# Kernel tuning notes

Measured on AMD Instinct MI355X. Metric: run time of the kernel, lower is better.

## Reference

```python
import jax, jax.numpy as jnp
import numpy as np

N = 100000        # number of nodes
E = 3200000       # number of edges (avg degree 32)
D_IN = 256
D_OUT = 256


def setup_inputs() -> dict:
    key = jax.random.key(0)
    k_x, k_w, k_r, k_c, k_v = jax.random.split(key, 5)
    x = jax.random.normal(k_x, (N, D_IN), dtype=jnp.float32)
    # nn.Linear weight, stored torch-style as (out_features, in_features)
    W = jax.random.normal(k_w, (D_OUT, D_IN), dtype=jnp.float32) / np.sqrt(D_IN)
    edge_row = jax.random.randint(k_r, (E,), 0, N, dtype=jnp.int32)
    edge_col = jax.random.randint(k_c, (E,), 0, N, dtype=jnp.int32)
    edge_val = jax.random.uniform(k_v, (E,), dtype=jnp.float32)
    return {"x": x, "W": W, "edge_row": edge_row, "edge_col": edge_col,
            "edge_val": edge_val}


def reference(x, W, edge_row, edge_col, edge_val):
    # support = X @ W^T  (torch nn.Linear, no bias), computed in float32
    support = jnp.einsum('nd,od->no', x.astype(jnp.float32), W.astype(jnp.float32))
    # SpMM: out[i] = sum_{e: row[e]==i} val[e] * support[col[e]]
    gathered = edge_val.astype(jnp.float32)[:, None] * support[edge_col]  # [E, D_OUT]
    out = jax.ops.segment_sum(gathered, edge_row, num_segments=N)        # [N, D_OUT]
    return out
```

## Files before the change

### kernel.cpp

```cpp
#include <hip/hip_runtime.h>

#define N_NODES 100000
#define N_EDGES 3200000
#define D 256

#define NBKT 391
#define BCAP 9216
#define P1_BLOCKS 782
#define GEMM_BLOCKS 1563
#define CVT_BLOCKS 64

using bf16x8 = __attribute__((ext_vector_type(8))) short;
using f32x4  = __attribute__((ext_vector_type(4))) float;
using i32x4  = __attribute__((ext_vector_type(4))) int;
using i32x2  = __attribute__((ext_vector_type(2))) int;

__device__ inline float bf2f(unsigned short b) {
    union { unsigned u; float f; } v; v.u = ((unsigned)b) << 16; return v.f;
}
__device__ inline unsigned short f2bf(float f) {
    union { float f; unsigned u; } v; v.f = f;
    unsigned u = v.u;
    u += 0x7FFFu + ((u >> 16) & 1u);
    return (unsigned short)(u >> 16);
}

__global__ __launch_bounds__(256) void prep(const float* __restrict__ W,
                                            unsigned short* __restrict__ wb,
                                            int* __restrict__ bucket_next) {
    int bid = blockIdx.x;
    if (bid < CVT_BLOCKS) {
        int i = (bid * 256 + threadIdx.x) * 4;
        float4 f = *(const float4*)(W + i);
        ushort4 o;
        o.x = f2bf(f.x); o.y = f2bf(f.y); o.z = f2bf(f.z); o.w = f2bf(f.w);
        *(ushort4*)(wb + i) = o;
    } else {
        int t = (bid - CVT_BLOCKS) * 256 + threadIdx.x;
        if (t < NBKT) bucket_next[t] = t * BCAP;
    }
}

__global__ __launch_bounds__(256) void gemm_part(
    const float* __restrict__ x,
    const unsigned short* __restrict__ wb,
    unsigned short* __restrict__ sb,
    const i32x4* __restrict__ erow4,
    const i32x4* __restrict__ ecol4,
    const f32x4* __restrict__ eval4,
    int* __restrict__ bucket_next,
    i32x2* __restrict__ bkt)
{
    __shared__ int h_cnt[NBKT];
    __shared__ int h_base[NBKT];
    int bid = blockIdx.x;
    int r3 = bid % 3, g3 = bid / 3;
    if (r3 == 0) {
        int p = g3;
        int tid = threadIdx.x;
        for (int i = tid; i < NBKT; i += 256) h_cnt[i] = 0;
        __syncthreads();
        int e0 = p * 4096;
        int jmax = (N_EDGES - e0) >> 10; if (jmax > 4) jmax = 4;
        int w0[4][4], w1[4][4], bs[4][4];
#pragma unroll
        for (int j = 0; j < 4; ++j) {
            if (j < jmax) {
                int q = p * 1024 + j * 256 + tid;
                i32x4 r4 = __builtin_nontemporal_load(erow4 + q);
                i32x4 c4 = __builtin_nontemporal_load(ecol4 + q);
                f32x4 v4 = __builtin_nontemporal_load(eval4 + q);
#pragma unroll
                for (int k = 0; k < 4; ++k) {
                    int row = r4[k];
                    int b   = row >> 8;
                    int rl  = row & 255;
                    int slot = atomicAdd(&h_cnt[b], 1);
                    w0[j][k] = c4[k] | (rl << 24);
                    w1[j][k] = __float_as_int(v4[k]);
                    bs[j][k] = (b << 14) | slot;
                }
            }
        }
        __syncthreads();
        for (int i = tid; i < NBKT; i += 256)
            h_base[i] = atomicAdd(&bucket_next[i], h_cnt[i]);
        __syncthreads();
#pragma unroll
        for (int j = 0; j < 4; ++j) {
            if (j < jmax) {
#pragma unroll
                for (int k = 0; k < 4; ++k) {
                    int b    = bs[j][k] >> 14;
                    int slot = bs[j][k] & 16383;
                    int dst  = h_base[b] + slot;
                    if (dst < (b + 1) * BCAP) {
                        i32x2 o; o[0] = w0[j][k]; o[1] = w1[j][k];
                        bkt[dst] = o;
                    }
                }
            }
        }
        return;
    }
    int g = 2 * g3 + (r3 - 1);
    int wave = g * 4 + (int)(threadIdx.x >> 6);
    int m0 = wave << 4;
    if (m0 >= N_NODES) return;
    int lane = threadIdx.x & 63;
    int quad = lane >> 4;
    int r16  = lane & 15;

    const f32x4* arow = (const f32x4*)(x + (size_t)(m0 + r16) * D + quad * 8);
    const unsigned short* bbase = wb + (size_t)r16 * D + quad * 8;

    f32x4 acc[16];
#pragma unroll
    for (int t = 0; t < 16; ++t) acc[t] = (f32x4){0.f, 0.f, 0.f, 0.f};

    for (int k0 = 0; k0 < D; k0 += 32) {
        f32x4 fa0 = __builtin_nontemporal_load(arow + (k0 >> 2));
        f32x4 fa1 = __builtin_nontemporal_load(arow + (k0 >> 2) + 1);
        bf16x8 a;
        a[0] = (short)f2bf(fa0[0]); a[1] = (short)f2bf(fa0[1]);
        a[2] = (short)f2bf(fa0[2]); a[3] = (short)f2bf(fa0[3]);
        a[4] = (short)f2bf(fa1[0]); a[5] = (short)f2bf(fa1[1]);
        a[6] = (short)f2bf(fa1[2]); a[7] = (short)f2bf(fa1[3]);
#pragma unroll
        for (int t = 0; t < 16; ++t) {
            bf16x8 b = *(const bf16x8*)(bbase + (size_t)t * 16 * D + k0);
            acc[t] = __builtin_amdgcn_mfma_f32_16x16x32_bf16(b, a, acc[t], 0, 0, 0);
        }
    }

#pragma unroll
    for (int t = 0; t < 16; ++t) {
        ushort4 o;
        o.x = f2bf(acc[t][0]); o.y = f2bf(acc[t][1]);
        o.z = f2bf(acc[t][2]); o.w = f2bf(acc[t][3]);
        *(ushort4*)(sb + (size_t)(m0 + r16) * D + t * 16 + quad * 4) = o;
    }
}

__global__ __launch_bounds__(1024) void build_csr(
    const int* __restrict__ bucket_next,
    i32x2* __restrict__ bkt,
    int* __restrict__ rowptr, int* __restrict__ cntout)
{
    __shared__ int cnt[256];
    __shared__ int scn[256];
    int b = blockIdx.x;
    int tid = threadIdx.x;
    int base = b * BCAP;
    int ne = bucket_next[b] - base; if (ne > BCAP) ne = BCAP;

    if (tid < 256) cnt[tid] = 0;
    __syncthreads();

    int w0[9], w1[9], sp[9];
#pragma unroll
    for (int j = 0; j < 9; ++j) {
        int idx = j * 1024 + tid;
        sp[j] = -1;
        if (idx < ne) {
            i32x2 e = bkt[base + idx];
            w0[j] = e[0]; w1[j] = e[1];
            int rl = ((unsigned)e[0]) >> 24;
            int s  = atomicAdd(&cnt[rl], 1);
            sp[j] = (rl << 16) | s;
        }
    }
    __syncthreads();
    if (tid < 256) scn[tid] = cnt[tid];
    __syncthreads();
    for (int off = 1; off < 256; off <<= 1) {
        int v = 0;
        if (tid < 256 && tid >= off) v = scn[tid - off];
        __syncthreads();
        if (tid < 256) scn[tid] += v;
        __syncthreads();
    }
    if (tid < 256) {
        int excl = scn[tid] - cnt[tid];
        scn[tid] = excl;
        int row = (b << 8) + tid;
        if (row < N_NODES) {
            rowptr[row] = base + excl;
            cntout[row] = cnt[tid];
        }
    }
    __syncthreads();
#pragma unroll
    for (int j = 0; j < 9; ++j) {
        if (sp[j] >= 0) {
            int rl = sp[j] >> 16, s = sp[j] & 0xFFFF;
            i32x2 o; o[0] = w0[j] & 0x00FFFFFF; o[1] = w1[j];
            bkt[base + scn[rl] + s] = o;
        }
    }
}

__global__ __launch_bounds__(256) void spmm_gather(
    const int* __restrict__ rowptr, const int* __restrict__ cntout,
    const i32x2* __restrict__ csr,
    const unsigned short* __restrict__ sb, float* __restrict__ out)
{
    int wave = (int)((blockIdx.x * 256u + threadIdx.x) >> 6);
    if (wave >= N_NODES) return;
    int lane = threadIdx.x & 63;
    int hi = lane >> 5;
    const unsigned short* base = sb + (size_t)(lane & 31) * 8;

    int beg = rowptr[wave];
    int end = beg + cntout[wave];

    f32x4 a0 = {0.f,0.f,0.f,0.f}, b0 = {0.f,0.f,0.f,0.f};
    f32x4 a1 = {0.f,0.f,0.f,0.f}, b1 = {0.f,0.f,0.f,0.f};
    f32x4 a2 = {0.f,0.f,0.f,0.f}, b2 = {0.f,0.f,0.f,0.f};
    f32x4 a3 = {0.f,0.f,0.f,0.f}, b3 = {0.f,0.f,0.f,0.f};

#define PAIR(AA, BB, EE) do {                                        \
        i32x2 pa = __builtin_nontemporal_load(csr + (EE));           \
        i32x2 pb = __builtin_nontemporal_load(csr + (EE) + 1);       \
        int   col = hi ? pb[0] : pa[0];                              \
        float v   = __int_as_float(hi ? pb[1] : pa[1]);              \
        bf16x8 s = *(const bf16x8*)(base + ((size_t)col << 8));      \
        AA[0] += v * bf2f((unsigned short)s[0]);                     \
        AA[1] += v * bf2f((unsigned short)s[1]);                     \
        AA[2] += v * bf2f((unsigned short)s[2]);                     \
        AA[3] += v * bf2f((unsigned short)s[3]);                     \
        BB[0] += v * bf2f((unsigned short)s[4]);                     \
        BB[1] += v * bf2f((unsigned short)s[5]);                     \
        BB[2] += v * bf2f((unsigned short)s[6]);                     \
        BB[3] += v * bf2f((unsigned short)s[7]);                     \
    } while (0)

    int e = beg;
    for (; e + 8 <= end; e += 8) {
        PAIR(a0, b0, e);
        PAIR(a1, b1, e + 2);
        PAIR(a2, b2, e + 4);
        PAIR(a3, b3, e + 6);
    }
    for (; e + 2 <= end; e += 2) PAIR(a0, b0, e);
    if (e < end) {
        i32x2 pa = __builtin_nontemporal_load(csr + e);
        int   col = pa[0];
        float v   = hi ? 0.f : __int_as_float(pa[1]);
        bf16x8 s = *(const bf16x8*)(base + ((size_t)col << 8));
        a0[0] += v * bf2f((unsigned short)s[0]);
        a0[1] += v * bf2f((unsigned short)s[1]);
        a0[2] += v * bf2f((unsigned short)s[2]);
        a0[3] += v * bf2f((unsigned short)s[3]);
        b0[0] += v * bf2f((unsigned short)s[4]);
        b0[1] += v * bf2f((unsigned short)s[5]);
        b0[2] += v * bf2f((unsigned short)s[6]);
        b0[3] += v * bf2f((unsigned short)s[7]);
    }
#undef PAIR

    f32x4 A = (a0 + a1) + (a2 + a3);
    f32x4 B = (b0 + b1) + (b2 + b3);
#pragma unroll
    for (int j = 0; j < 4; ++j) {
        A[j] += __shfl_xor(A[j], 32);
        B[j] += __shfl_xor(B[j], 32);
    }
    if (lane < 32) {
        float* o = out + (size_t)wave * D + lane * 8;
        __builtin_nontemporal_store(A, (f32x4*)o);
        __builtin_nontemporal_store(B, (f32x4*)(o + 4));
    }
}

extern "C" void kernel_launch(void* const* d_in, const int* in_sizes, int n_in,
                              void* d_out, int out_size, void* d_ws, size_t ws_size,
                              hipStream_t stream) {
    const float* x    = (const float*)d_in[0];
    const float* W    = (const float*)d_in[1];
    const int*   erow = (const int*)d_in[2];
    const int*   ecol = (const int*)d_in[3];
    const float* eval = (const float*)d_in[4];
    float* out = (float*)d_out;

    char* ws = (char*)d_ws;
    unsigned short* wb     = (unsigned short*)(ws + 0);
    unsigned short* sb     = (unsigned short*)(ws + 131072);
    int*            bnext  = (int*)(ws + 51331072);
    int*            rowptr = (int*)(ws + 51335168);
    int*            cnt    = (int*)(ws + 51735168);
    i32x2*          bkt    = (i32x2*)(ws + 52135168);

    prep<<<CVT_BLOCKS + 2, 256, 0, stream>>>(W, wb, bnext);

    gemm_part<<<3 * P1_BLOCKS, 256, 0, stream>>>(
        x, wb, sb, (const i32x4*)erow, (const i32x4*)ecol, (const f32x4*)eval,
        bnext, bkt);

    build_csr<<<NBKT, 1024, 0, stream>>>(bnext, bkt, rowptr, cnt);

    spmm_gather<<<N_NODES / 4, 256, 0, stream>>>(rowptr, cnt, bkt, sb, out);
}
```

Baseline: 583.6 us.

## Fuse CSR build and SpMM gather into one kernel using LDS-staged buckets

Halves the bucket size to 128 rows and merges the bucket-sort kernel with the gather kernel. Each block counting-sorts its bucket's edges into shared memory and then processes its rows directly. This removes one launch, the global write-back of sorted edges, and the rowptr/count arrays. The cost is fewer, larger blocks with serial per-wave row loops and a sizable LDS footprint, which may reduce latency hiding in the gather.

```diff
diff --git a/kernel.cpp b/kernel.cpp
--- a/kernel.cpp
+++ b/kernel.cpp
@@ -4,10 +4,9 @@
 #define N_EDGES 3200000
 #define D 256
 
-#define NBKT 391
-#define BCAP 9216
+#define NBKT 782
+#define BCAP 4608
 #define P1_BLOCKS 782
-#define GEMM_BLOCKS 1563
 #define CVT_BLOCKS 64
 
 using bf16x8 = __attribute__((ext_vector_type(8))) short;
@@ -73,12 +72,12 @@
 #pragma unroll
                 for (int k = 0; k < 4; ++k) {
                     int row = r4[k];
-                    int b   = row >> 8;
-                    int rl  = row & 255;
+                    int b   = row >> 7;
+                    int rl  = row & 127;
                     int slot = atomicAdd(&h_cnt[b], 1);
                     w0[j][k] = c4[k] | (rl << 24);
                     w1[j][k] = __float_as_int(v4[k]);
-                    bs[j][k] = (b << 14) | slot;
+                    bs[j][k] = (b << 13) | slot;
                 }
             }
         }
@@ -91,8 +90,8 @@
             if (j < jmax) {
 #pragma unroll
                 for (int k = 0; k < 4; ++k) {
-                    int b    = bs[j][k] >> 14;
-                    int slot = bs[j][k] & 16383;
+                    int b    = bs[j][k] >> 13;
+                    int slot = bs[j][k] & 8191;
                     int dst  = h_base[b] + slot;
                     if (dst < (b + 1) * BCAP) {
                         i32x2 o; o[0] = w0[j][k]; o[1] = w1[j][k];
@@ -142,89 +141,52 @@
     }
 }
 
-__global__ __launch_bounds__(1024) void build_csr(
+__global__ __launch_bounds__(512) void csr_spmm(
     const int* __restrict__ bucket_next,
-    i32x2* __restrict__ bkt,
-    int* __restrict__ rowptr, int* __restrict__ cntout)
+    const i32x2* __restrict__ bkt,
+    const unsigned short* __restrict__ sb, float* __restrict__ out)
 {
-    __shared__ int cnt[256];
-    __shared__ int scn[256];
-    int b = blockIdx.x;
-    int tid = threadIdx.x;
+    __shared__ int2 lds_e[BCAP];
+    __shared__ int cnt[128], scn[128], cur[128];
+    int b = blockIdx.x, tid = threadIdx.x;
     int base = b * BCAP;
     int ne = bucket_next[b] - base; if (ne > BCAP) ne = BCAP;
 
-    if (tid < 256) cnt[tid] = 0;
-    __syncthreads();
-
-    int w0[9], w1[9], sp[9];
-#pragma unroll
-    for (int j = 0; j < 9; ++j) {
-        int idx = j * 1024 + tid;
-        sp[j] = -1;
-        if (idx < ne) {
-            i32x2 e = bkt[base + idx];
-            w0[j] = e[0]; w1[j] = e[1];
-            int rl = ((unsigned)e[0]) >> 24;
-            int s  = atomicAdd(&cnt[rl], 1);
-            sp[j] = (rl << 16) | s;
-        }
-    }
-    __syncthreads();
-    if (tid < 256) scn[tid] = cnt[tid];
-    __syncthreads();
-    for (int off = 1; off < 256; off <<= 1) {
+    if (tid < 128) cnt[tid] = 0;
+    __syncthreads();
+    for (int idx = tid; idx < ne; idx += 512) {
+        i32x2 e = bkt[base + idx];
+        atomicAdd(&cnt[((unsigned)e[0]) >> 24], 1);
+    }
+    __syncthreads();
+    if (tid < 128) scn[tid] = cnt[tid];
+    __syncthreads();
+    for (int off = 1; off < 128; off <<= 1) {
         int v = 0;
-        if (tid < 256 && tid >= off) v = scn[tid - off];
-        __syncthreads();
-        if (tid < 256) scn[tid] += v;
-        __syncthreads();
-    }
-    if (tid < 256) {
-        int excl = scn[tid] - cnt[tid];
-        scn[tid] = excl;
-        int row = (b << 8) + tid;
-        if (row < N_NODES) {
-            rowptr[row] = base + excl;
-            cntout[row] = cnt[tid];
-        }
-    }
-    __syncthreads();
-#pragma unroll
-    for (int j = 0; j < 9; ++j) {
-        if (sp[j] >= 0) {
-            int rl = sp[j] >> 16, s = sp[j] & 0xFFFF;
-            i32x2 o; o[0] = w0[j] & 0x00FFFFFF; o[1] = w1[j];
-            bkt[base + scn[rl] + s] = o;
-        }
-    }
-}
-
-__global__ __launch_bounds__(256) void spmm_gather(
-    const int* __restrict__ rowptr, const int* __restrict__ cntout,
-    const i32x2* __restrict__ csr,
-    const unsigned short* __restrict__ sb, float* __restrict__ out)
-{
-    int wave = (int)((blockIdx.x * 256u + threadIdx.x) >> 6);
-    if (wave >= N_NODES) return;
-    int lane = threadIdx.x & 63;
-    int hi = lane >> 5;
-    const unsigned short* base = sb + (size_t)(lane & 31) * 8;
-
-    int beg = rowptr[wave];
-    int end = beg + cntout[wave];
-
-    f32x4 a0 = {0.f,0.f,0.f,0.f}, b0 = {0.f,0.f,0.f,0.f};
-    f32x4 a1 = {0.f,0.f,0.f,0.f}, b1 = {0.f,0.f,0.f,0.f};
-    f32x4 a2 = {0.f,0.f,0.f,0.f}, b2 = {0.f,0.f,0.f,0.f};
-    f32x4 a3 = {0.f,0.f,0.f,0.f}, b3 = {0.f,0.f,0.f,0.f};
+        if (tid < 128 && tid >= off) v = scn[tid - off];
+        __syncthreads();
+        if (tid < 128) scn[tid] += v;
+        __syncthreads();
+    }
+    if (tid < 128) { int ex = scn[tid] - cnt[tid]; scn[tid] = ex; cur[tid] = ex; }
+    __syncthreads();
+    for (int idx = tid; idx < ne; idx += 512) {
+        i32x2 e = bkt[base + idx];
+        int rl  = ((unsigned)e[0]) >> 24;
+        int pos = atomicAdd(&cur[rl], 1);
+        lds_e[pos] = make_int2(e[0] & 0x00FFFFFF, e[1]);
+    }
+    __syncthreads();
+
+    int wid = tid >> 6, lane = tid & 63, hi = lane >> 5;
+    const unsigned short* basep = sb + (size_t)(lane & 31) * 8;
 
 #define PAIR(AA, BB, EE) do {                                        \
-        i32x2 pa = __builtin_nontemporal_load(csr + (EE));           \
-        i32x2 pb = __builtin_nontemporal_load(csr + (EE) + 1);       \
-        int   col = hi ? pb[0] : pa[0];                              \
-        float v   = __int_as_float(hi ? pb[1] : pa[1]);              \
-        bf16x8 s = *(const bf16x8*)(base + ((size_t)col << 8));      \
+        int2 pa = lds_e[EE];                                         \
+        int2 pb = lds_e[(EE) + 1];                                   \
+        int   col = hi ? pb.x : pa.x;                                \
+        float v   = __int_as_float(hi ? pb.y : pa.y);                \
+        bf16x8 s = *(const bf16x8*)(basep + ((size_t)col << 8));     \
         AA[0] += v * bf2f((unsigned short)s[0]);                     \
         AA[1] += v * bf2f((unsigned short)s[1]);                     \
         AA[2] += v * bf2f((unsigned short)s[2]);                     \
@@ -235,42 +197,54 @@
         BB[3] += v * bf2f((unsigned short)s[7]);                     \
     } while (0)
 
-    int e = beg;
-    for (; e + 8 <= end; e += 8) {
-        PAIR(a0, b0, e);
-        PAIR(a1, b1, e + 2);
-        PAIR(a2, b2, e + 4);
-        PAIR(a3, b3, e + 6);
-    }
-    for (; e + 2 <= end; e += 2) PAIR(a0, b0, e);
-    if (e < end) {
-        i32x2 pa = __builtin_nontemporal_load(csr + e);
-        int   col = pa[0];
-        float v   = hi ? 0.f : __int_as_float(pa[1]);
-        bf16x8 s = *(const bf16x8*)(base + ((size_t)col << 8));
-        a0[0] += v * bf2f((unsigned short)s[0]);
-        a0[1] += v * bf2f((unsigned short)s[1]);
-        a0[2] += v * bf2f((unsigned short)s[2]);
-        a0[3] += v * bf2f((unsigned short)s[3]);
-        b0[0] += v * bf2f((unsigned short)s[4]);
-        b0[1] += v * bf2f((unsigned short)s[5]);
-        b0[2] += v * bf2f((unsigned short)s[6]);
-        b0[3] += v * bf2f((unsigned short)s[7]);
+    for (int r = 0; r < 16; ++r) {
+        int rl  = wid * 16 + r;
+        int row = (b << 7) + rl;
+        if (row >= N_NODES) break;
+        int e   = scn[rl];
+        int end = cur[rl];
+
+        f32x4 a0 = {0.f,0.f,0.f,0.f}, b0 = {0.f,0.f,0.f,0.f};
+        f32x4 a1 = {0.f,0.f,0.f,0.f}, b1 = {0.f,0.f,0.f,0.f};
+        f32x4 a2 = {0.f,0.f,0.f,0.f}, b2 = {0.f,0.f,0.f,0.f};
+        f32x4 a3 = {0.f,0.f,0.f,0.f}, b3 = {0.f,0.f,0.f,0.f};
+
+        for (; e + 8 <= end; e += 8) {
+            PAIR(a0, b0, e);
+            PAIR(a1, b1, e + 2);
+            PAIR(a2, b2, e + 4);
+            PAIR(a3, b3, e + 6);
+        }
+        for (; e + 2 <= end; e += 2) PAIR(a0, b0, e);
+        if (e < end) {
+            int2 pa = lds_e[e];
+            int   col = pa.x;
+            float v   = hi ? 0.f : __int_as_float(pa.y);
+            bf16x8 s = *(const bf16x8*)(basep + ((size_t)col << 8));
+            a0[0] += v * bf2f((unsigned short)s[0]);
+            a0[1] += v * bf2f((unsigned short)s[1]);
+            a0[2] += v * bf2f((unsigned short)s[2]);
+            a0[3] += v * bf2f((unsigned short)s[3]);
+            b0[0] += v * bf2f((unsigned short)s[4]);
+            b0[1] += v * bf2f((unsigned short)s[5]);
+            b0[2] += v * bf2f((unsigned short)s[6]);
+            b0[3] += v * bf2f((unsigned short)s[7]);
+        }
+
+        f32x4 A = (a0 + a1) + (a2 + a3);
+        f32x4 B = (b0 + b1) + (b2 + b3);
+#pragma unroll
+        for (int j = 0; j < 4; ++j) {
+            A[j] += __shfl_xor(A[j], 32);
+            B[j] += __shfl_xor(B[j], 32);
+        }
+        if (lane < 32) {
+            float* o = out + (size_t)row * D + lane * 8;
+            __builtin_nontemporal_store(A, (f32x4*)o);
+            __builtin_nontemporal_store(B, (f32x4*)(o + 4));
+        }
     }
 #undef PAIR
-
-    f32x4 A = (a0 + a1) + (a2 + a3);
-    f32x4 B = (b0 + b1) + (b2 + b3);
-#pragma unroll
-    for (int j = 0; j < 4; ++j) {
-        A[j] += __shfl_xor(A[j], 32);
-        B[j] += __shfl_xor(B[j], 32);
-    }
-    if (lane < 32) {
-        float* o = out + (size_t)wave * D + lane * 8;
-        __builtin_nontemporal_store(A, (f32x4*)o);
-        __builtin_nontemporal_store(B, (f32x4*)(o + 4));
-    }
 }
 
 extern "C" void kernel_launch(void* const* d_in, const int* in_sizes, int n_in,
@@ -284,20 +258,16 @@
     float* out = (float*)d_out;
 
     char* ws = (char*)d_ws;
-    unsigned short* wb     = (unsigned short*)(ws + 0);
-    unsigned short* sb     = (unsigned short*)(ws + 131072);
-    int*            bnext  = (int*)(ws + 51331072);
-    int*            rowptr = (int*)(ws + 51335168);
-    int*            cnt    = (int*)(ws + 51735168);
-    i32x2*          bkt    = (i32x2*)(ws + 52135168);
-
-    prep<<<CVT_BLOCKS + 2, 256, 0, stream>>>(W, wb, bnext);
+    unsigned short* wb    = (unsigned short*)(ws + 0);
+    unsigned short* sb    = (unsigned short*)(ws + 131072);
+    int*            bnext = (int*)(ws + 51331072);
+    i32x2*          bkt   = (i32x2*)(ws + 51335168);
+
+    prep<<<CVT_BLOCKS + 4, 256, 0, stream>>>(W, wb, bnext);
 
     gemm_part<<<3 * P1_BLOCKS, 256, 0, stream>>>(
         x, wb, sb, (const i32x4*)erow, (const i32x4*)ecol, (const f32x4*)eval,
         bnext, bkt);
 
-    build_csr<<<NBKT, 1024, 0, stream>>>(bnext, bkt, rowptr, cnt);
-
-    spmm_gather<<<N_NODES / 4, 256, 0, stream>>>(rowptr, cnt, bkt, sb, out);
-}
+    csr_spmm<<<NBKT, 512, 0, stream>>>(bnext, bkt, sb, out);
+}
```

After: 565.6 us. 3.1% less time.
